# Kernel tuning notes

Measured on AMD Instinct MI355X. Metric: run time of the kernel, lower is better.

Reference implementation:

```python
import jax, jax.numpy as jnp
import numpy as np

EPS = 1e-5
DN = ('NCHW', 'OIHW', 'NCHW')


def _conv(x, w):
    return jax.lax.conv_general_dilated(x, w, (1, 1), 'SAME', dimension_numbers=DN)


def _bn(x, g, b, m, v):
    # eval-mode batchnorm over channel axis 1
    inv = jax.lax.rsqrt(v + EPS)
    return (x - m[:, None, None]) * (g * inv)[:, None, None] + b[:, None, None]


def setup_inputs() -> dict:
    key = jax.random.key(0)
    ks = jax.random.split(key, 32)
    dim, mid, B, H, W = 256, 128, 4, 128, 128
    d = {}
    d['x'] = jax.random.normal(ks[0], (B, dim, H, W), dtype=jnp.float32)

    def bn_params(i, c):
        return (jax.random.uniform(ks[i], (c,), dtype=jnp.float32) + 0.5,
                jax.random.normal(ks[i + 1], (c,), dtype=jnp.float32) * 0.1,
                jax.random.normal(ks[i + 2], (c,), dtype=jnp.float32) * 0.1,
                jax.random.uniform(ks[i + 3], (c,), dtype=jnp.float32) + 0.5)

    d['w_p1'] = jax.random.normal(ks[1], (mid, dim, 3, 3), dtype=jnp.float32) * 0.02
    d['g_p1'], d['b_p1'], d['m_p1'], d['v_p1'] = bn_params(2, mid)
    d['w_p2'] = jax.random.normal(ks[6], (mid, dim, 3, 3), dtype=jnp.float32) * 0.02
    d['g_p2'], d['b_p2'], d['m_p2'], d['v_p2'] = bn_params(7, mid)
    d['w_c1'] = jax.random.normal(ks[11], (dim, mid, 3, 3), dtype=jnp.float32) * 0.02
    d['g_c1'], d['b_c1'], d['m_c1'], d['v_c1'] = bn_params(12, dim)
    d['w_c2'] = jax.random.normal(ks[16], (dim, dim, 1, 1), dtype=jnp.float32) * 0.02
    d['g_c2'], d['b_c2'], d['m_c2'], d['v_c2'] = bn_params(17, dim)
    d['w_p3'] = jax.random.normal(ks[21], (dim, dim, 3, 3), dtype=jnp.float32) * 0.02
    d['g_p3'], d['b_p3'], d['m_p3'], d['v_p3'] = bn_params(22, dim)
    return d


def reference(x,
              w_p1, g_p1, b_p1, m_p1, v_p1,
              w_p2, g_p2, b_p2, m_p2, v_p2,
              w_c1, g_c1, b_c1, m_c1, v_c1,
              w_c2, g_c2, b_c2, m_c2, v_c2,
              w_p3, g_p3, b_p3, m_p3, v_p3):
    # conv-bn-relu branches (dim -> 128)
    p1 = jax.nn.relu(_bn(_conv(x, w_p1), g_p1, b_p1, m_p1, v_p1))
    p2 = jax.nn.relu(_bn(_conv(x, w_p2), g_p2, b_p2, m_p2, v_p2))
    # corner pooling: 'top' = reverse cummax over H (axis 2),
    #                 'left' = reverse cummax over W (axis 3)
    cp1 = jax.lax.cummax(p1, axis=2, reverse=True)
    cp2 = jax.lax.cummax(p2, axis=3, reverse=True)
    bn1 = _bn(_conv(cp1 + cp2, w_c1), g_c1, b_c1, m_c1, v_c1)
    bn2 = _bn(_conv(x, w_c2), g_c2, b_c2, m_c2, v_c2)
    r = jax.nn.relu(bn1 + bn2)
    out = jax.nn.relu(_bn(_conv(r, w_p3), g_p3, b_p3, m_p3, v_p3))
    return out
```

## Files before the change

kernel.cpp:

```cpp
#include <hip/hip_runtime.h>
#include <math.h>

#define HH 128
#define WW 128
#define HWSZ (128*128)

typedef __attribute__((ext_vector_type(8))) short short8;
typedef __attribute__((ext_vector_type(4))) float float4v;

__device__ inline short f2bf(float f) {
  unsigned x = __float_as_uint(f);
  unsigned r = (x + 0x7fffu + ((x >> 16) & 1u)) >> 16;
  return (short)r;
}
__device__ inline float bf2f(unsigned short u) {
  return __uint_as_float(((unsigned)u) << 16);
}
__device__ inline int swz(int row, int g) {
  return row * 32 + ((g ^ ((row >> 1) & 3)) << 3);
}

__global__ __launch_bounds__(256) void xcvt_kernel(const float* __restrict__ x,
                                                   short* __restrict__ xbf) {
  __shared__ short tile[32 * 264];
  const int t = threadIdx.x;
  const int h = blockIdx.x, b = blockIdx.y;
  for (int wc = 0; wc < 4; wc++) {
    const int w0 = wc * 32;
    __syncthreads();
    #pragma unroll
    for (int coi = 0; coi < 8; coi++) {
      int ci = coi * 32 + (t >> 3);
      int wq = t & 7;
      float4v f = *(const float4v*)&x[((size_t)b * 256 + ci) * HWSZ + h * WW + w0 + wq * 4];
      tile[(wq * 4 + 0) * 264 + ci] = f2bf(f.x);
      tile[(wq * 4 + 1) * 264 + ci] = f2bf(f.y);
      tile[(wq * 4 + 2) * 264 + ci] = f2bf(f.z);
      tile[(wq * 4 + 3) * 264 + ci] = f2bf(f.w);
    }
    __syncthreads();
    #pragma unroll
    for (int pass = 0; pass < 4; pass++) {
      int wl = pass * 8 + (t >> 5);
      int ci8 = (t & 31) * 8;
      short8 v = *(const short8*)&tile[wl * 264 + ci8];
      *(short8*)&xbf[(((size_t)b * HH + h) * WW + w0 + wl) * 256 + ci8] = v;
    }
  }
}

__global__ void wcvt3_kernel(const float* __restrict__ w, const float* __restrict__ g,
                             const float* __restrict__ v, short* __restrict__ out,
                             int Cin, int CoutW, int co_off) {
  int idx = blockIdx.x * blockDim.x + threadIdx.x;
  int total = CoutW * Cin * 9;
  if (idx >= total) return;
  int t  = idx % 9;
  int ci = (idx / 9) % Cin;
  int co = idx / (9 * Cin);
  float s = g[co] * rsqrtf(v[co] + 1e-5f);
  out[((size_t)t * 256 + co_off + co) * Cin + ci] = f2bf(w[idx] * s);
}

__global__ void wcvt1_kernel(const float* __restrict__ w, const float* __restrict__ g,
                             const float* __restrict__ v, short* __restrict__ out,
                             int Cin, int CoutW) {
  int idx = blockIdx.x * blockDim.x + threadIdx.x;
  if (idx >= CoutW * Cin) return;
  int co = idx / Cin;
  float s = g[co] * rsqrtf(v[co] + 1e-5f);
  out[idx] = f2bf(w[idx] * s);
}

template<int CIN_A, bool PHASE_B, int SHIFT_MODE, bool SPLIT_OUT, bool OUT_F32>
__global__ __launch_bounds__(256, 2) void conv_mfma(
    const short* __restrict__ srcA, const short* __restrict__ xB,
    const short* __restrict__ wbA, const short* __restrict__ wbB,
    const float* __restrict__ g0, const float* __restrict__ b0,
    const float* __restrict__ m0, const float* __restrict__ v0,
    const float* __restrict__ g1, const float* __restrict__ b1,
    const float* __restrict__ m1, const float* __restrict__ v1,
    void* __restrict__ out0, void* __restrict__ out1)
{
  __shared__ short A_s[130 * 32];
  __shared__ short B_s[3 * 256 * 32];

  const int tid  = threadIdx.x;
  const int wave = tid >> 6;
  const int lane = tid & 63;
  const int wm = wave & 1;
  const int wn = wave >> 1;
  const int lr = lane & 15;
  const int lk = lane >> 4;

  const int h  = blockIdx.x & 127;
  const int b  = blockIdx.x >> 7;

  constexpr int ncA = CIN_A / 32;
  const int dystart = (h == 0) ? 1 : 0;
  const int dyend   = (h == HH - 1) ? 2 : 3;
  const int chunksA = (dyend - dystart) * ncA;
  const int total   = chunksA + (PHASE_B ? 8 : 0);

  float4v acc[4][8];
  #pragma unroll
  for (int i = 0; i < 4; i++)
    #pragma unroll
    for (int j = 0; j < 8; j++) acc[i][j] = (float4v)(0.0f);

  short8 rA[3], rB[12];
  const short* aRow = nullptr;
  const short* bBase = nullptr;
  bool curIsA = true;

  auto decode = [&](int t, const short*& ar, const short*& bb, bool& isA) {
    isA = (t < chunksA);
    if (isA) {
      int dy  = dystart + t / ncA;
      int ci0 = (t % ncA) * 32;
      ar = srcA + (((size_t)b * HH + (h + dy - 1)) * WW) * CIN_A + ci0;
      bb = wbA + ((size_t)(dy * 3) * 256) * CIN_A + ci0;
    } else {
      int ci0 = (t - chunksA) * 32;
      ar = xB + (((size_t)b * HH + h) * WW) * 256 + ci0;
      bb = wbB + ci0;
    }
  };

  auto loadRegs = [&](const short* ar, const short* bb, bool isA) {
    if (isA) {
      #pragma unroll
      for (int i = 0; i < 2; i++) {
        int idx = tid + i * 256;
        int w = (idx >> 2) - 1, q = idx & 3;
        rA[i] = ((unsigned)w < (unsigned)WW)
                  ? *(const short8*)(ar + (size_t)w * CIN_A + q * 8) : (short8)(0);
      }
      if (tid < 8) {
        int idx = tid + 512;
        int w = (idx >> 2) - 1, q = idx & 3;
        rA[2] = ((unsigned)w < (unsigned)WW)
                  ? *(const short8*)(ar + (size_t)w * CIN_A + q * 8) : (short8)(0);
      }
      #pragma unroll
      for (int i = 0; i < 12; i++) {
        int idx = tid + i * 256;
        int dx = idx >> 10, rem = idx & 1023;
        int co = rem >> 2, q = rem & 3;
        rB[i] = *(const short8*)(bb + (size_t)(dx * 256 + co) * CIN_A + q * 8);
      }
    } else {
      #pragma unroll
      for (int i = 0; i < 2; i++) {
        int idx = tid + i * 256;
        int wp = idx >> 2, q = idx & 3;
        rA[i] = *(const short8*)(ar + (size_t)wp * 256 + q * 8);
      }
      #pragma unroll
      for (int i = 0; i < 4; i++) {
        int idx = tid + i * 256;
        int co = idx >> 2, q = idx & 3;
        rB[i] = *(const short8*)(bb + (size_t)co * 256 + q * 8);
      }
    }
  };

  auto storeLDS = [&](bool isA) {
    if (isA) {
      #pragma unroll
      for (int i = 0; i < 2; i++) {
        int idx = tid + i * 256;
        *(short8*)&A_s[swz(idx >> 2, idx & 3)] = rA[i];
      }
      if (tid < 8) {
        int idx = tid + 512;
        *(short8*)&A_s[swz(idx >> 2, idx & 3)] = rA[2];
      }
      #pragma unroll
      for (int i = 0; i < 12; i++) {
        int idx = tid + i * 256;
        int dx = idx >> 10, rem = idx & 1023;
        *(short8*)&B_s[swz(dx * 256 + (rem >> 2), rem & 3)] = rB[i];
      }
    } else {
      #pragma unroll
      for (int i = 0; i < 2; i++) {
        int idx = tid + i * 256;
        *(short8*)&A_s[swz(idx >> 2, idx & 3)] = rA[i];
      }
      #pragma unroll
      for (int i = 0; i < 4; i++) {
        int idx = tid + i * 256;
        *(short8*)&B_s[swz(idx >> 2, idx & 3)] = rB[i];
      }
    }
  };

  decode(0, aRow, bBase, curIsA);
  loadRegs(aRow, bBase, curIsA);

  for (int t = 0; t < total; t++) {
    bool isA = curIsA;
    __syncthreads();
    storeLDS(isA);
    __syncthreads();
    if (t + 1 < total) {
      decode(t + 1, aRow, bBase, curIsA);
      loadRegs(aRow, bBase, curIsA);
    }
    const int ndx = isA ? 3 : 1;
    for (int dx = 0; dx < ndx; dx++) {
      short8 af[4];
      #pragma unroll
      for (int mi = 0; mi < 4; mi++)
        af[mi] = *(const short8*)&A_s[swz(wm * 64 + mi * 16 + lr + dx, lk)];
      #pragma unroll
      for (int ni = 0; ni < 8; ni++) {
        short8 bfr = *(const short8*)&B_s[swz(dx * 256 + wn * 128 + ni * 16 + lr, lk)];
        #pragma unroll
        for (int mi = 0; mi < 4; mi++)
          acc[mi][ni] = __builtin_amdgcn_mfma_f32_16x16x32_bf16(af[mi], bfr, acc[mi][ni], 0, 0, 0);
      }
    }
  }

  #pragma unroll
  for (int ni = 0; ni < 8; ni++) {
    int c = wn * 128 + ni * 16 + lr;
    float sh;
    if (SHIFT_MODE == 0) {
      float s = g0[c] * rsqrtf(v0[c] + 1e-5f);
      sh = b0[c] - m0[c] * s;
    } else if (SHIFT_MODE == 1) {
      int cc = c & 127;
      const float* gg = (c < 128) ? g0 : g1;
      const float* bb = (c < 128) ? b0 : b1;
      const float* mm = (c < 128) ? m0 : m1;
      const float* vv = (c < 128) ? v0 : v1;
      float s = gg[cc] * rsqrtf(vv[cc] + 1e-5f);
      sh = bb[cc] - mm[cc] * s;
    } else {
      float s0 = g0[c] * rsqrtf(v0[c] + 1e-5f);
      float s1 = g1[c] * rsqrtf(v1[c] + 1e-5f);
      sh = (b0[c] - m0[c] * s0) + (b1[c] - m1[c] * s1);
    }
    #pragma unroll
    for (int mi = 0; mi < 4; mi++) {
      int px = wm * 64 + mi * 16 + lk * 4;
      float4v v = acc[mi][ni];
      v.x = fmaxf(v.x + sh, 0.0f);
      v.y = fmaxf(v.y + sh, 0.0f);
      v.z = fmaxf(v.z + sh, 0.0f);
      v.w = fmaxf(v.w + sh, 0.0f);
      if (OUT_F32) {
        float* ob = (float*)out0;
        *(float4v*)(ob + ((size_t)b * 256 + c) * HWSZ + (size_t)h * WW + px) = v;
      } else if (SPLIT_OUT) {
        short* ob = (short*)((c < 128) ? out0 : out1);
        size_t base = (((size_t)b * HH + h) * WW + px) * 128 + (c & 127);
        ob[base      ] = f2bf(v.x);
        ob[base + 128 ] = f2bf(v.y);
        ob[base + 256 ] = f2bf(v.z);
        ob[base + 384 ] = f2bf(v.w);
      } else {
        short* ob = (short*)out0;
        size_t base = (((size_t)b * HH + h) * WW + px) * 256 + c;
        ob[base      ] = f2bf(v.x);
        ob[base + 256 ] = f2bf(v.y);
        ob[base + 512 ] = f2bf(v.z);
        ob[base + 768 ] = f2bf(v.w);
      }
    }
  }
}

__global__ void colscan_kernel(unsigned* __restrict__ p) {
  const int t = threadIdx.x;
  const int wl = t >> 6, cp = t & 63;
  const int w = blockIdx.x * 4 + wl;
  const int b = blockIdx.y;
  float m0 = -INFINITY, m1 = -INFINITY;
  for (int h = HH - 1; h >= 0; h--) {
    size_t idx = (((size_t)b * HH + h) * WW + w) * 64 + cp;
    unsigned u = p[idx];
    float f0 = bf2f((unsigned short)(u & 0xffff));
    float f1 = bf2f((unsigned short)(u >> 16));
    m0 = fmaxf(m0, f0);
    m1 = fmaxf(m1, f1);
    p[idx] = ((unsigned)(unsigned short)f2bf(m1) << 16) | (unsigned short)f2bf(m0);
  }
}

__global__ __launch_bounds__(256) void rowscan_add_kernel(
    const short* __restrict__ p2, short* __restrict__ p1) {
  __shared__ short pl[128 * 128];
  const int tid = threadIdx.x;
  const int hb = blockIdx.x;
  const int b  = blockIdx.y;
  const size_t base = (((size_t)b * HH + hb) * WW) * 128;

  #pragma unroll
  for (int i = 0; i < 8; i++) {
    int idx = tid + i * 256;
    *(short8*)&pl[idx * 8] = *(const short8*)(p2 + base + (size_t)idx * 8);
  }
  __syncthreads();
  if (tid < 128) {
    float m = -INFINITY;
    for (int w = WW - 1; w >= 0; w--) {
      int a = w * 128 + tid;
      m = fmaxf(m, bf2f((unsigned short)pl[a]));
      pl[a] = (short)f2bf(m);
    }
  }
  __syncthreads();
  #pragma unroll
  for (int i = 0; i < 8; i++) {
    int idx = tid + i * 256;
    short8 sv = *(const short8*)&pl[idx * 8];
    short8 ov = *(const short8*)(p1 + base + (size_t)idx * 8);
    short8 rv;
    #pragma unroll
    for (int j = 0; j < 8; j++)
      rv[j] = f2bf(bf2f((unsigned short)sv[j]) + bf2f((unsigned short)ov[j]));
    *(short8*)(p1 + base + (size_t)idx * 8) = rv;
  }
}

extern "C" void kernel_launch(void* const* d_in, const int* in_sizes, int n_in,
                              void* d_out, int out_size, void* d_ws, size_t ws_size,
                              hipStream_t stream) {
  const float* x    = (const float*)d_in[0];
  const float* w_p1 = (const float*)d_in[1];
  const float* g_p1 = (const float*)d_in[2];
  const float* b_p1 = (const float*)d_in[3];
  const float* m_p1 = (const float*)d_in[4];
  const float* v_p1 = (const float*)d_in[5];
  const float* w_p2 = (const float*)d_in[6];
  const float* g_p2 = (const float*)d_in[7];
  const float* b_p2 = (const float*)d_in[8];
  const float* m_p2 = (const float*)d_in[9];
  const float* v_p2 = (const float*)d_in[10];
  const float* w_c1 = (const float*)d_in[11];
  const float* g_c1 = (const float*)d_in[12];
  const float* b_c1 = (const float*)d_in[13];
  const float* m_c1 = (const float*)d_in[14];
  const float* v_c1 = (const float*)d_in[15];
  const float* w_c2 = (const float*)d_in[16];
  const float* g_c2 = (const float*)d_in[17];
  const float* b_c2 = (const float*)d_in[18];
  const float* m_c2 = (const float*)d_in[19];
  const float* v_c2 = (const float*)d_in[20];
  const float* w_p3 = (const float*)d_in[21];
  const float* g_p3 = (const float*)d_in[22];
  const float* b_p3 = (const float*)d_in[23];
  const float* m_p3 = (const float*)d_in[24];
  const float* v_p3 = (const float*)d_in[25];

  char* ws = (char*)d_ws;
  short* p1  = (short*)(ws + 0);
  short* p2  = (short*)(ws + 16777216);
  short* r   = (short*)(ws + 33554432);
  short* xbf = (short*)(ws + 67108864);
  short* wb12 = r;
  short* wbc1 = p2;
  short* wbc2 = (short*)(ws + 16777216 + 589824);
  short* wbp3 = p1;

  xcvt_kernel<<<dim3(128, 4), 256, 0, stream>>>(x, xbf);

  wcvt3_kernel<<<(128 * 256 * 9 + 255) / 256, 256, 0, stream>>>(w_p1, g_p1, v_p1, wb12, 256, 128, 0);
  wcvt3_kernel<<<(128 * 256 * 9 + 255) / 256, 256, 0, stream>>>(w_p2, g_p2, v_p2, wb12, 256, 128, 128);

  conv_mfma<256, false, 1, true, false><<<dim3(512), 256, 0, stream>>>(
      xbf, nullptr, wb12, nullptr,
      g_p1, b_p1, m_p1, v_p1, g_p2, b_p2, m_p2, v_p2, (void*)p1, (void*)p2);

  colscan_kernel<<<dim3(32, 4), 256, 0, stream>>>((unsigned*)p1);
  rowscan_add_kernel<<<dim3(128, 4), 256, 0, stream>>>(p2, p1);

  wcvt3_kernel<<<(256 * 128 * 9 + 255) / 256, 256, 0, stream>>>(w_c1, g_c1, v_c1, wbc1, 128, 256, 0);
  wcvt1_kernel<<<(256 * 256 + 255) / 256, 256, 0, stream>>>(w_c2, g_c2, v_c2, wbc2, 256, 256);

  conv_mfma<128, true, 2, false, false><<<dim3(512), 256, 0, stream>>>(
      p1, xbf, wbc1, wbc2,
      g_c1, b_c1, m_c1, v_c1, g_c2, b_c2, m_c2, v_c2, (void*)r, nullptr);

  wcvt3_kernel<<<(256 * 256 * 9 + 255) / 256, 256, 0, stream>>>(w_p3, g_p3, v_p3, wbp3, 256, 256, 0);

  conv_mfma<256, false, 0, false, true><<<dim3(512), 256, 0, stream>>>(
      r, nullptr, wbp3, nullptr,
      g_p3, b_p3, m_p3, v_p3, nullptr, nullptr, nullptr, nullptr, d_out, nullptr);
}
```

Measured before the change: 425.7 us.

## Merge prep kernels and split column cummax scan into two parallel halves

Fuses the input transpose/convert with the two first-stage weight conversions into one launch, and likewise merges the second-stage weight conversions, cutting four launches down to two. The column reverse-cummax scan now splits each column into two 64-row halves handled by separate thread groups. The lower half is buffered in registers and fixed up with the upper half's running max through shared memory. This doubles the parallelism of a latency-bound serial scan, at the cost of a 64-entry register array and an extra barrier.

```diff
diff --git a/kernel.cpp b/kernel.cpp
--- a/kernel.cpp
+++ b/kernel.cpp
@@ -20,32 +20,68 @@
   return row * 32 + ((g ^ ((row >> 1) & 3)) << 3);
 }
 
-__global__ __launch_bounds__(256) void xcvt_kernel(const float* __restrict__ x,
-                                                   short* __restrict__ xbf) {
+__global__ __launch_bounds__(256) void prep1_kernel(
+    const float* __restrict__ x, short* __restrict__ xbf,
+    const float* __restrict__ w_p1, const float* __restrict__ g_p1, const float* __restrict__ v_p1,
+    const float* __restrict__ w_p2, const float* __restrict__ g_p2, const float* __restrict__ v_p2,
+    short* __restrict__ wb12) {
   __shared__ short tile[32 * 264];
+  const int bid = blockIdx.x;
   const int t = threadIdx.x;
-  const int h = blockIdx.x, b = blockIdx.y;
-  for (int wc = 0; wc < 4; wc++) {
-    const int w0 = wc * 32;
-    __syncthreads();
-    #pragma unroll
-    for (int coi = 0; coi < 8; coi++) {
-      int ci = coi * 32 + (t >> 3);
-      int wq = t & 7;
-      float4v f = *(const float4v*)&x[((size_t)b * 256 + ci) * HWSZ + h * WW + w0 + wq * 4];
-      tile[(wq * 4 + 0) * 264 + ci] = f2bf(f.x);
-      tile[(wq * 4 + 1) * 264 + ci] = f2bf(f.y);
-      tile[(wq * 4 + 2) * 264 + ci] = f2bf(f.z);
-      tile[(wq * 4 + 3) * 264 + ci] = f2bf(f.w);
-    }
-    __syncthreads();
-    #pragma unroll
-    for (int pass = 0; pass < 4; pass++) {
-      int wl = pass * 8 + (t >> 5);
-      int ci8 = (t & 31) * 8;
-      short8 v = *(const short8*)&tile[wl * 264 + ci8];
-      *(short8*)&xbf[(((size_t)b * HH + h) * WW + w0 + wl) * 256 + ci8] = v;
-    }
+  if (bid < 512) {
+    const int h = bid & 127, b = bid >> 7;
+    for (int wc = 0; wc < 4; wc++) {
+      const int w0 = wc * 32;
+      __syncthreads();
+      #pragma unroll
+      for (int coi = 0; coi < 8; coi++) {
+        int ci = coi * 32 + (t >> 3);
+        int wq = t & 7;
+        float4v f = *(const float4v*)&x[((size_t)b * 256 + ci) * HWSZ + h * WW + w0 + wq * 4];
+        tile[(wq * 4 + 0) * 264 + ci] = f2bf(f.x);
+        tile[(wq * 4 + 1) * 264 + ci] = f2bf(f.y);
+        tile[(wq * 4 + 2) * 264 + ci] = f2bf(f.z);
+        tile[(wq * 4 + 3) * 264 + ci] = f2bf(f.w);
+      }
+      __syncthreads();
+      #pragma unroll
+      for (int pass = 0; pass < 4; pass++) {
+        int wl = pass * 8 + (t >> 5);
+        int ci8 = (t & 31) * 8;
+        short8 v = *(const short8*)&tile[wl * 264 + ci8];
+        *(short8*)&xbf[(((size_t)b * HH + h) * WW + w0 + wl) * 256 + ci8] = v;
+      }
+    }
+  } else {
+    int e = (bid - 512) * 256 + t;
+    if (e >= 589824) return;
+    const float* w; const float* g; const float* v; int co_off;
+    if (e < 294912) { w = w_p1; g = g_p1; v = v_p1; co_off = 0; }
+    else { e -= 294912; w = w_p2; g = g_p2; v = v_p2; co_off = 128; }
+    int t9 = e % 9;
+    int ci = (e / 9) & 255;
+    int co = e / (9 * 256);
+    float s = g[co] * rsqrtf(v[co] + 1e-5f);
+    wb12[((size_t)t9 * 256 + co_off + co) * 256 + ci] = f2bf(w[e] * s);
+  }
+}
+
+__global__ __launch_bounds__(256) void prep2_kernel(
+    const float* __restrict__ w_c1, const float* __restrict__ g_c1, const float* __restrict__ v_c1,
+    const float* __restrict__ w_c2, const float* __restrict__ g_c2, const float* __restrict__ v_c2,
+    short* __restrict__ wbc1, short* __restrict__ wbc2) {
+  int e = blockIdx.x * 256 + threadIdx.x;
+  if (e < 294912) {
+    int t9 = e % 9;
+    int ci = (e / 9) & 127;
+    int co = e / (9 * 128);
+    float s = g_c1[co] * rsqrtf(v_c1[co] + 1e-5f);
+    wbc1[((size_t)t9 * 256 + co) * 128 + ci] = f2bf(w_c1[e] * s);
+  } else if (e < 360448) {
+    int e2 = e - 294912;
+    int co = e2 >> 8;
+    float s = g_c2[co] * rsqrtf(v_c2[co] + 1e-5f);
+    wbc2[e2] = f2bf(w_c2[e2] * s);
   }
 }
 
@@ -60,16 +96,6 @@
   int co = idx / (9 * Cin);
   float s = g[co] * rsqrtf(v[co] + 1e-5f);
   out[((size_t)t * 256 + co_off + co) * Cin + ci] = f2bf(w[idx] * s);
-}
-
-__global__ void wcvt1_kernel(const float* __restrict__ w, const float* __restrict__ g,
-                             const float* __restrict__ v, short* __restrict__ out,
-                             int Cin, int CoutW) {
-  int idx = blockIdx.x * blockDim.x + threadIdx.x;
-  if (idx >= CoutW * Cin) return;
-  int co = idx / Cin;
-  float s = g[co] * rsqrtf(v[co] + 1e-5f);
-  out[idx] = f2bf(w[idx] * s);
 }
 
 template<int CIN_A, bool PHASE_B, int SHIFT_MODE, bool SPLIT_OUT, bool OUT_F32>
@@ -274,20 +300,48 @@
   }
 }
 
-__global__ void colscan_kernel(unsigned* __restrict__ p) {
+__global__ __launch_bounds__(256) void colscan_kernel(unsigned* __restrict__ p) {
+  __shared__ float sm[2][2][64];
   const int t = threadIdx.x;
-  const int wl = t >> 6, cp = t & 63;
-  const int w = blockIdx.x * 4 + wl;
+  const int wl = t >> 7, seg = (t >> 6) & 1, cp = t & 63;
+  const int w = blockIdx.x * 2 + wl;
   const int b = blockIdx.y;
+  const size_t colbase = ((size_t)b * HH * WW + w) * 64 + cp;
   float m0 = -INFINITY, m1 = -INFINITY;
-  for (int h = HH - 1; h >= 0; h--) {
-    size_t idx = (((size_t)b * HH + h) * WW + w) * 64 + cp;
-    unsigned u = p[idx];
-    float f0 = bf2f((unsigned short)(u & 0xffff));
-    float f1 = bf2f((unsigned short)(u >> 16));
-    m0 = fmaxf(m0, f0);
-    m1 = fmaxf(m1, f1);
-    p[idx] = ((unsigned)(unsigned short)f2bf(m1) << 16) | (unsigned short)f2bf(m0);
+  unsigned r[64];
+  if (seg) {
+    #pragma unroll
+    for (int i = 0; i < 64; i++) {
+      int h = 127 - i;
+      size_t idx = colbase + (size_t)h * (WW * 64);
+      unsigned u = p[idx];
+      m0 = fmaxf(m0, bf2f((unsigned short)(u & 0xffff)));
+      m1 = fmaxf(m1, bf2f((unsigned short)(u >> 16)));
+      p[idx] = ((unsigned)(unsigned short)f2bf(m1) << 16) | (unsigned short)f2bf(m0);
+    }
+    sm[wl][0][cp] = m0;
+    sm[wl][1][cp] = m1;
+  } else {
+    #pragma unroll
+    for (int i = 0; i < 64; i++) {
+      int h = 63 - i;
+      unsigned u = p[colbase + (size_t)h * (WW * 64)];
+      m0 = fmaxf(m0, bf2f((unsigned short)(u & 0xffff)));
+      m1 = fmaxf(m1, bf2f((unsigned short)(u >> 16)));
+      r[i] = ((unsigned)(unsigned short)f2bf(m1) << 16) | (unsigned short)f2bf(m0);
+    }
+  }
+  __syncthreads();
+  if (!seg) {
+    float b0 = sm[wl][0][cp], b1 = sm[wl][1][cp];
+    #pragma unroll
+    for (int i = 0; i < 64; i++) {
+      int h = 63 - i;
+      float f0 = fmaxf(bf2f((unsigned short)(r[i] & 0xffff)), b0);
+      float f1 = fmaxf(bf2f((unsigned short)(r[i] >> 16)), b1);
+      p[colbase + (size_t)h * (WW * 64)] =
+          ((unsigned)(unsigned short)f2bf(f1) << 16) | (unsigned short)f2bf(f0);
+    }
   }
 }
 
@@ -367,20 +421,18 @@
   short* wbc2 = (short*)(ws + 16777216 + 589824);
   short* wbp3 = p1;
 
-  xcvt_kernel<<<dim3(128, 4), 256, 0, stream>>>(x, xbf);
-
-  wcvt3_kernel<<<(128 * 256 * 9 + 255) / 256, 256, 0, stream>>>(w_p1, g_p1, v_p1, wb12, 256, 128, 0);
-  wcvt3_kernel<<<(128 * 256 * 9 + 255) / 256, 256, 0, stream>>>(w_p2, g_p2, v_p2, wb12, 256, 128, 128);
+  prep1_kernel<<<dim3(2816), 256, 0, stream>>>(x, xbf,
+      w_p1, g_p1, v_p1, w_p2, g_p2, v_p2, wb12);
 
   conv_mfma<256, false, 1, true, false><<<dim3(512), 256, 0, stream>>>(
       xbf, nullptr, wb12, nullptr,
       g_p1, b_p1, m_p1, v_p1, g_p2, b_p2, m_p2, v_p2, (void*)p1, (void*)p2);
 
-  colscan_kernel<<<dim3(32, 4), 256, 0, stream>>>((unsigned*)p1);
+  colscan_kernel<<<dim3(64, 4), 256, 0, stream>>>((unsigned*)p1);
   rowscan_add_kernel<<<dim3(128, 4), 256, 0, stream>>>(p2, p1);
 
-  wcvt3_kernel<<<(256 * 128 * 9 + 255) / 256, 256, 0, stream>>>(w_c1, g_c1, v_c1, wbc1, 128, 256, 0);
-  wcvt1_kernel<<<(256 * 256 + 255) / 256, 256, 0, stream>>>(w_c2, g_c2, v_c2, wbc2, 256, 256);
+  prep2_kernel<<<dim3(1408), 256, 0, stream>>>(
+      w_c1, g_c1, v_c1, w_c2, g_c2, v_c2, wbc1, wbc2);
 
   conv_mfma<128, true, 2, false, false><<<dim3(512), 256, 0, stream>>>(
       p1, xbf, wbc1, wbc2,
```

Measured after the change: 416.0 us. 1.02x faster.
